# Optimization experiments

Measured on AMD Instinct MI355X. Metric: run time of the kernel, lower is better.

The kernel has to match this reference:

```python
import jax, jax.numpy as jnp
import numpy as np

N, D, K = 131072, 64, 1024


def setup_inputs() -> dict:
    key = jax.random.key(0)
    kx, kc = jax.random.split(key)
    x = jax.random.normal(kx, (N, D), dtype=jnp.float32)
    # codebook ~ trunc_normal(std=0.2); plain normal*0.2 is a faithful stand-in
    codebook = 0.2 * jax.random.normal(kc, (K, D), dtype=jnp.float32)
    temperature = jnp.ones((1,), dtype=jnp.float32)
    return {"x": x, "codebook": codebook, "temperature": temperature}


def reference(x, codebook, temperature):
    # squared euclidean distances: [N, K]
    dist = (
        jnp.sum(x * x, axis=1, keepdims=True)
        + jnp.sum(codebook * codebook, axis=1)[None, :]
        - 2.0 * (x @ codebook.T)
    )
    neg_dist = -dist
    ids = jnp.argmax(neg_dist, axis=1)  # nearest code per row
    # Note: original tests `if self.train:` (a bound method, always truthy),
    # so the gumbel-softmax branch always executes.
    gkey = jax.random.key(42)
    g = jax.random.gumbel(gkey, neg_dist.shape, dtype=neg_dist.dtype)
    weights = jax.nn.softmax((neg_dist + g) / temperature[0], axis=-1)  # [N, K]
    emb = weights @ codebook  # [N, D]
    return emb, ids
```

## Files before the change

### kernel.cpp

```cpp
#include <hip/hip_runtime.h>
#include <stdint.h>

#define N_ROWS 131072
#define DIM 64
#define K_CODES 1024

typedef __attribute__((ext_vector_type(8))) short short8;
typedef __attribute__((ext_vector_type(4))) float float4v;
typedef __attribute__((ext_vector_type(4))) uint32_t u32x4;

#define LOG2E 1.4426950408889634f
#define LOG2_LN2 -0.5287663729448977f

__device__ __forceinline__ uint32_t cvt_pk_bf16(float lo, float hi) {
    uint32_t r;
    asm("v_cvt_pk_bf16_f32 %0, %1, %2" : "=v"(r) : "v"(lo), "v"(hi));
    return r;
}
__device__ __forceinline__ uint32_t lo_pack(float fe, float fo, uint32_t h) {
    float le = fe - __uint_as_float(h << 16);
    float lo_ = fo - __uint_as_float(h & 0xffff0000u);
    return cvt_pk_bf16(le, lo_);
}
__device__ __forceinline__ float exp2_fast(float x) {
    float r; asm("v_exp_f32 %0, %1" : "=v"(r) : "v"(x)); return r;
}
__device__ __forceinline__ float log2_fast(float x) {
    float r; asm("v_log_f32 %0, %1" : "=v"(r) : "v"(x)); return r;
}

__device__ __forceinline__ void dma16(const void* g, void* l) {
    __builtin_amdgcn_global_load_lds(
        (const __attribute__((address_space(1))) uint32_t*)g,
        (__attribute__((address_space(3))) uint32_t*)l,
        16, 0, 0);
}

template<int V> struct IC { static constexpr int v = V; };

__global__ __launch_bounds__(256) void nscale_kernel(const float* __restrict__ cb,
                                                     const float* __restrict__ temp,
                                                     float* __restrict__ nsc) {
    int k = blockIdx.x * 256 + threadIdx.x;
    if (k < K_CODES) {
        const float invT = 1.0f / temp[0];
        const float* r = cb + k * DIM;
        float s = 0.f;
        #pragma unroll
        for (int j = 0; j < DIM; ++j) s = fmaf(r[j], r[j], s);
        nsc[k] = fmaf(s, -invT * LOG2E, -LOG2_LN2);
    }
}

__global__ __launch_bounds__(256) void cbimg_kernel(const float* __restrict__ cb,
                                                    const float* __restrict__ temp,
                                                    uint16_t* __restrict__ img) {
    const int tile = blockIdx.x, tid = threadIdx.x;
    const int code = tid & 31, db = (tid >> 5) * 8;
    const int k = tile * 32 + code;
    const float sc = (1.0f / temp[0]) * LOG2E;
    const float4* src = reinterpret_cast<const float4*>(cb + (size_t)k * DIM + db);
    const float4 a = src[0], b = src[1];
    uint32_t h0 = cvt_pk_bf16(a.x, a.y), h1 = cvt_pk_bf16(a.z, a.w);
    uint32_t h2 = cvt_pk_bf16(b.x, b.y), h3 = cvt_pk_bf16(b.z, b.w);
    const float sax = a.x*sc, say = a.y*sc, saz = a.z*sc, saw = a.w*sc;
    const float sbx = b.x*sc, sby = b.y*sc, sbz = b.z*sc, sbw = b.w*sc;
    uint32_t g0 = cvt_pk_bf16(sax, say), g1 = cvt_pk_bf16(saz, saw);
    uint32_t g2 = cvt_pk_bf16(sbx, sby), g3 = cvt_pk_bf16(sbz, sbw);
    u32x4 hv = {g0, g1, g2, g3};
    u32x4 lv = { lo_pack(sax,say,g0), lo_pack(saz,saw,g1),
                 lo_pack(sbx,sby,g2), lo_pack(sbz,sbw,g3) };
    uint16_t* t = img + (size_t)tile * 7168;
    *(u32x4*)&t[code*72 + db]        = hv;
    *(u32x4*)&t[2304 + code*72 + db] = lv;
    const int pc = ((code & 15) << 1) | (code >> 4);
    t[4608 + (db+0)*40 + pc] = (uint16_t)h0;
    t[4608 + (db+1)*40 + pc] = (uint16_t)(h0 >> 16);
    t[4608 + (db+2)*40 + pc] = (uint16_t)h1;
    t[4608 + (db+3)*40 + pc] = (uint16_t)(h1 >> 16);
    t[4608 + (db+4)*40 + pc] = (uint16_t)h2;
    t[4608 + (db+5)*40 + pc] = (uint16_t)(h2 >> 16);
    t[4608 + (db+6)*40 + pc] = (uint16_t)h3;
    t[4608 + (db+7)*40 + pc] = (uint16_t)(h3 >> 16);
}

__device__ __forceinline__ uint32_t rotl32(uint32_t x, uint32_t r) {
    return __builtin_amdgcn_alignbit(x, x, 32u - r);
}
__device__ __forceinline__ void tf_round4(uint32_t x0[4], uint32_t x1[4], uint32_t r) {
    #pragma unroll
    for (int i = 0; i < 4; ++i) { x0[i] += x1[i]; x1[i] = rotl32(x1[i], r); x1[i] ^= x0[i]; }
}
__device__ __forceinline__ void threefry4w_k42(const uint32_t c0[4],
                                               uint32_t o0[4], uint32_t o1[4]) {
    const uint32_t ks1 = 42u, ks2 = 0x1BD11BDAu ^ 42u;
    uint32_t x0[4], x1[4];
    #pragma unroll
    for (int i = 0; i < 4; ++i) { x0[i] = c0[i]; x1[i] = c0[i] + (1u<<26) + ks1; }
    tf_round4(x0,x1,13); tf_round4(x0,x1,15); tf_round4(x0,x1,26); tf_round4(x0,x1,6);
    #pragma unroll
    for (int i = 0; i < 4; ++i) { x0[i] += ks1; x1[i] += ks2 + 1u; }
    tf_round4(x0,x1,17); tf_round4(x0,x1,29); tf_round4(x0,x1,16); tf_round4(x0,x1,24);
    #pragma unroll
    for (int i = 0; i < 4; ++i) { x0[i] += ks2; x1[i] += 2u; }
    tf_round4(x0,x1,13); tf_round4(x0,x1,15); tf_round4(x0,x1,26); tf_round4(x0,x1,6);
    #pragma unroll
    for (int i = 0; i < 4; ++i) { x1[i] += ks1 + 3u; }
    tf_round4(x0,x1,17); tf_round4(x0,x1,29); tf_round4(x0,x1,16); tf_round4(x0,x1,24);
    #pragma unroll
    for (int i = 0; i < 4; ++i) { x0[i] += ks1; x1[i] += ks2 + 4u; }
    tf_round4(x0,x1,13); tf_round4(x0,x1,15); tf_round4(x0,x1,26); tf_round4(x0,x1,6);
    #pragma unroll
    for (int i = 0; i < 4; ++i) { o0[i] = x0[i] + ks2; o1[i] = x1[i] + 5u; }
}

__device__ __forceinline__ float gumbel_l(uint32_t bits) {
    uint32_t fb = __builtin_amdgcn_alignbit(0x7Fu, bits, 9u);
    return log2_fast(__uint_as_float(fb) - 1.0f);
}

template<bool T1>
__device__ __forceinline__ void quant_body(
    const float* __restrict__ x, const uint16_t* __restrict__ img,
    const float* __restrict__ cb, const float invT,
    float* __restrict__ out_emb, float* __restrict__ out_ids,
    char* smem, const float* __restrict__ nscg)
{
    uint16_t* const xhiP  = (uint16_t*)smem;
    uint16_t* const xloP  = (uint16_t*)(smem + 9216);
    uint16_t* const pbufP = (uint16_t*)(smem + 28672);
    float*    const nscLDS = (float*)(smem + 33792);

    const int tid  = threadIdx.x;
    const int wave = tid >> 6, lane = tid & 63, quad = lane >> 4, col = lane & 15;
    const int rowbase = blockIdx.x * 32 + wave * 8;

    {
        const int s = tid >> 2, w = s >> 4, t = s & 15, dq = tid & 3;
        const int row = blockIdx.x * 32 + w * 8 + (t >> 1) + ((t & 1) << 16);
        const float4* src = reinterpret_cast<const float4*>(x + (size_t)row * DIM + dq * 16);
        float4 f0 = src[0], f1 = src[1], f2 = src[2], f3 = src[3];
        u32x4 hA = { cvt_pk_bf16(f0.x,f0.y), cvt_pk_bf16(f0.z,f0.w),
                     cvt_pk_bf16(f1.x,f1.y), cvt_pk_bf16(f1.z,f1.w) };
        u32x4 hB = { cvt_pk_bf16(f2.x,f2.y), cvt_pk_bf16(f2.z,f2.w),
                     cvt_pk_bf16(f3.x,f3.y), cvt_pk_bf16(f3.z,f3.w) };
        u32x4 lA = { lo_pack(f0.x,f0.y,hA[0]), lo_pack(f0.z,f0.w,hA[1]),
                     lo_pack(f1.x,f1.y,hA[2]), lo_pack(f1.z,f1.w,hA[3]) };
        u32x4 lB = { lo_pack(f2.x,f2.y,hB[0]), lo_pack(f2.z,f2.w,hB[1]),
                     lo_pack(f3.x,f3.y,hB[2]), lo_pack(f3.z,f3.w,hB[3]) };
        uint16_t* dsth = &xhiP[(w*16 + t)*72 + dq*16];
        uint16_t* dstl = &xloP[(w*16 + t)*72 + dq*16];
        *(u32x4*)(dsth)     = hA;
        *(u32x4*)(dsth + 8) = hB;
        *(u32x4*)(dstl)     = lA;
        *(u32x4*)(dstl + 8) = lB;
    }
    __syncthreads();

    const int arb = (wave*16 + col)*72;
    const short8 ahi0 = *(const short8*)&xhiP[arb + quad*8];
    const short8 ahi1 = *(const short8*)&xhiP[arb + 32 + quad*8];
    const short8 alo0 = *(const short8*)&xloP[arb + quad*8];
    const short8 alo1 = *(const short8*)&xloP[arb + 32 + quad*8];
    __syncthreads();

    const char* gdma = (const char*)img + (size_t)lane * 16;
    auto dma_tile = [&](int tile, int bofs) {
        const char* s = gdma + (size_t)tile * 14336;
        char* d = smem + bofs;
        dma16(s + (size_t)wave*1024,     d + wave*1024);
        dma16(s + (size_t)(wave+4)*1024, d + (wave+4)*1024);
        dma16(s + (size_t)(wave+8)*1024, d + (wave+8)*1024);
        if (wave < 2) dma16(s + (size_t)(wave+12)*1024, d + (wave+12)*1024);
    };
    dma_tile(0, 0);
    dma16((const char*)nscg + (size_t)wave*1024 + (size_t)lane*16,
          smem + 33792 + wave*1024);
    __syncthreads();

    const uint32_t base_c0 = (uint32_t)(rowbase + 2*quad) * 1024u + (uint32_t)col;

    float m[4]  = {-1e30f, -1e30f, -1e30f, -1e30f};
    float Zp[4] = {0.f, 0.f, 0.f, 0.f};
    float4v e0 = {0,0,0,0}, e1 = {0,0,0,0}, e2 = {0,0,0,0}, e3 = {0,0,0,0};
    float zt[4] = {-3.4e38f,-3.4e38f,-3.4e38f,-3.4e38f};
    float zs[4] = {-3.4e38f,-3.4e38f,-3.4e38f,-3.4e38f};
    int   kt[4] = {0,0,0,0}, ks[4] = {0,0,0,0};

    auto body = [&](int blk, auto B) {
        constexpr int BOF = decltype(B)::v;
        const uint16_t* cbhi = (const uint16_t*)(smem + BOF);
        const uint16_t* cblo = cbhi + 2304;
        const uint16_t* cbT  = cbhi + 4608;
        const int kb  = blk * 32;
        const int kc0 = kb + col, kc1 = kc0 + 16;

        if (blk + 1 < 32) dma_tile(blk + 1, BOF ^ 14336);
        const float nsc0 = nscLDS[kc0], nsc1 = nscLDS[kc1];

        float l0c[4], l1c[4];
        {
            const uint32_t cA = base_c0 + (uint32_t)kb;
            const uint32_t c0s[4] = {cA, cA + 1024u, cA + 16u, cA + 1040u};
            uint32_t o0[4], o1[4];
            threefry4w_k42(c0s, o0, o1);
            float l[8];
            #pragma unroll
            for (int i = 0; i < 4; ++i) { l[2*i] = gumbel_l(o0[i]); l[2*i+1] = gumbel_l(o1[i]); }
            #pragma unroll
            for (int j = 0; j < 4; ++j) {
                if (T1) { l0c[j] = l[j]; l1c[j] = l[4+j]; }
                else {
                    l0c[j] = -invT * (log2_fast(-l[j])   + LOG2_LN2);
                    l1c[j] = -invT * (log2_fast(-l[4+j]) + LOG2_LN2);
                }
            }
        }

        float4v S0 = {0,0,0,0}, S1 = {0,0,0,0};
        {
            const int rb0 = col*72;
            const short8 bh0 = *(const short8*)&cbhi[rb0 + quad*8];
            const short8 bh1 = *(const short8*)&cbhi[rb0 + 32 + quad*8];
            const short8 bl0 = *(const short8*)&cblo[rb0 + quad*8];
            const short8 bl1 = *(const short8*)&cblo[rb0 + 32 + quad*8];
            S0 = __builtin_amdgcn_mfma_f32_16x16x32_bf16(ahi0, bh0, S0, 0,0,0);
            S0 = __builtin_amdgcn_mfma_f32_16x16x32_bf16(ahi1, bh1, S0, 0,0,0);
            S0 = __builtin_amdgcn_mfma_f32_16x16x32_bf16(ahi0, bl0, S0, 0,0,0);
            S0 = __builtin_amdgcn_mfma_f32_16x16x32_bf16(ahi1, bl1, S0, 0,0,0);
            S0 = __builtin_amdgcn_mfma_f32_16x16x32_bf16(alo0, bh0, S0, 0,0,0);
            S0 = __builtin_amdgcn_mfma_f32_16x16x32_bf16(alo1, bh1, S0, 0,0,0);
        }
        {
            const int rb1 = (16 + col)*72;
            const short8 bh0 = *(const short8*)&cbhi[rb1 + quad*8];
            const short8 bh1 = *(const short8*)&cbhi[rb1 + 32 + quad*8];
            const short8 bl0 = *(const short8*)&cblo[rb1 + quad*8];
            const short8 bl1 = *(const short8*)&cblo[rb1 + 32 + quad*8];
            S1 = __builtin_amdgcn_mfma_f32_16x16x32_bf16(ahi0, bh0, S1, 0,0,0);
            S1 = __builtin_amdgcn_mfma_f32_16x16x32_bf16(ahi1, bh1, S1, 0,0,0);
            S1 = __builtin_amdgcn_mfma_f32_16x16x32_bf16(ahi0, bl0, S1, 0,0,0);
            S1 = __builtin_amdgcn_mfma_f32_16x16x32_bf16(ahi1, bl1, S1, 0,0,0);
            S1 = __builtin_amdgcn_mfma_f32_16x16x32_bf16(alo0, bh0, S1, 0,0,0);
            S1 = __builtin_amdgcn_mfma_f32_16x16x32_bf16(alo1, bh1, S1, 0,0,0);
        }

        float z0v[4], z1v[4];
        #pragma unroll
        for (int j = 0; j < 4; ++j) {
            const float z0 = fmaf(S0[j], 2.0f, nsc0);
            const float z1 = fmaf(S1[j], 2.0f, nsc1);
            {   const bool c1 = z0 > zt[j], c2 = z0 > zs[j];
                const float zsn = __builtin_amdgcn_fmed3f(z0, zt[j], zs[j]);
                ks[j] = c1 ? kt[j] : (c2 ? kc0 : ks[j]);
                kt[j] = c1 ? kc0 : kt[j];
                zt[j] = fmaxf(zt[j], z0);
                zs[j] = zsn; }
            {   const bool c1 = z1 > zt[j], c2 = z1 > zs[j];
                const float zsn = __builtin_amdgcn_fmed3f(z1, zt[j], zs[j]);
                ks[j] = c1 ? kt[j] : (c2 ? kc1 : ks[j]);
                kt[j] = c1 ? kc1 : kt[j];
                zt[j] = fmaxf(zt[j], z1);
                zs[j] = zsn; }
            z0v[j] = z0; z1v[j] = z1;
        }

        if (T1) {
            #pragma unroll
            for (int j = 0; j < 4; ++j) {
                const float p0 = exp2_fast(z0v[j]) * __builtin_amdgcn_rcpf(-l0c[j]);
                const float p1 = exp2_fast(z1v[j]) * __builtin_amdgcn_rcpf(-l1c[j]);
                Zp[j] += p0 + p1;
                ((uint32_t*)pbufP)[(wave*16 + quad*4 + j)*20 + col] = cvt_pk_bf16(p0, p1);
            }
        } else {
            float a0[4], a1[4], zm[4];
            #pragma unroll
            for (int j = 0; j < 4; ++j) {
                a0[j] = z0v[j] + l0c[j];
                a1[j] = z1v[j] + l1c[j];
                zm[j] = fmaxf(a0[j], a1[j]);
            }
            float4v av;
            #pragma unroll
            for (int j = 0; j < 4; ++j) {
                float mn = fmaxf(m[j], zm[j]);
                #pragma unroll
                for (int mask = 1; mask < 16; mask <<= 1)
                    mn = fmaxf(mn, __shfl_xor(mn, mask));
                const float al = exp2_fast(m[j] - mn);
                m[j] = mn; Zp[j] *= al; av[j] = al;
            }
            e0 *= av; e1 *= av; e2 *= av; e3 *= av;
            #pragma unroll
            for (int j = 0; j < 4; ++j) {
                const float p0 = exp2_fast(a0[j] - m[j]);
                const float p1 = exp2_fast(a1[j] - m[j]);
                Zp[j] += p0 + p1;
                ((uint32_t*)pbufP)[(wave*16 + quad*4 + j)*20 + col] = cvt_pk_bf16(p0, p1);
            }
        }

        const short8 pa  = *(const short8*)&pbufP[(wave*16 + col)*40 + quad*8];
        const short8 bt0 = *(const short8*)&cbT[( 0 + col)*40 + quad*8];
        const short8 bt1 = *(const short8*)&cbT[(16 + col)*40 + quad*8];
        const short8 bt2 = *(const short8*)&cbT[(32 + col)*40 + quad*8];
        const short8 bt3 = *(const short8*)&cbT[(48 + col)*40 + quad*8];
        e0 = __builtin_amdgcn_mfma_f32_16x16x32_bf16(pa, bt0, e0, 0,0,0);
        e1 = __builtin_amdgcn_mfma_f32_16x16x32_bf16(pa, bt1, e1, 0,0,0);
        e2 = __builtin_amdgcn_mfma_f32_16x16x32_bf16(pa, bt2, e2, 0,0,0);
        e3 = __builtin_amdgcn_mfma_f32_16x16x32_bf16(pa, bt3, e3, 0,0,0);

        __syncthreads();
    };

    for (int blk = 0; blk < 32; blk += 2) {
        body(blk,     IC<0>{});
        body(blk + 1, IC<14336>{});
    }

    #pragma unroll
    for (int mask = 1; mask < 16; mask <<= 1) {
        #pragma unroll
        for (int j = 0; j < 4; ++j) Zp[j] += __shfl_xor(Zp[j], mask);
    }
    #pragma unroll
    for (int mask = 1; mask < 16; mask <<= 1) {
        #pragma unroll
        for (int j = 0; j < 4; ++j) {
            const float ozt = __shfl_xor(zt[j], mask);
            const float ozs = __shfl_xor(zs[j], mask);
            const int   okt = __shfl_xor(kt[j], mask);
            const int   oks = __shfl_xor(ks[j], mask);
            const bool mf = (zt[j] > ozt) || (zt[j] == ozt && kt[j] < okt);
            const float w1 = mf ? zt[j] : ozt;  const int wk1 = mf ? kt[j] : okt;
            const float l1 = mf ? ozt : zt[j];  const int lk1 = mf ? okt : kt[j];
            const float w2 = mf ? zs[j] : ozs;  const int wk2 = mf ? ks[j] : oks;
            const bool s1 = (l1 > w2) || (l1 == w2 && lk1 < wk2);
            zt[j] = w1; kt[j] = wk1;
            zs[j] = s1 ? l1 : w2; ks[j] = s1 ? lk1 : wk2;
        }
    }
    if (col == 0) {
        #pragma unroll
        for (int j = 0; j < 4; ++j) {
            if (zt[j] - zs[j] < 0.015f * invT) {
                const int t = quad*4 + j;
                const int row = rowbase + (t >> 1) + ((t & 1) << 16);
                const float* xr = x + (size_t)row * DIM;
                const float* cA = cb + (size_t)kt[j] * DIM;
                const float* cB = cb + (size_t)ks[j] * DIM;
                double dA = 0.0, dB = 0.0;
                for (int d = 0; d < DIM; ++d) {
                    const double xv = (double)xr[d];
                    const double av2 = (double)cA[d], bv = (double)cB[d];
                    dA = fma(av2, av2, dA); dA = fma(-2.0*xv, av2, dA);
                    dB = fma(bv,  bv,  dB); dB = fma(-2.0*xv, bv,  dB);
                }
                if (dB < dA || (dB == dA && ks[j] < kt[j])) kt[j] = ks[j];
            }
        }
    }
    #pragma unroll
    for (int j = 0; j < 4; ++j) {
        const int t = quad*4 + j;
        const int row = rowbase + (t >> 1) + ((t & 1) << 16);
        const float rZ = __builtin_amdgcn_rcpf(Zp[j]);
        out_emb[(size_t)row * DIM +      col] = e0[j] * rZ;
        out_emb[(size_t)row * DIM + 16 + col] = e1[j] * rZ;
        out_emb[(size_t)row * DIM + 32 + col] = e2[j] * rZ;
        out_emb[(size_t)row * DIM + 48 + col] = e3[j] * rZ;
        if (col == 0) out_ids[row] = (float)kt[j];
    }
}

__global__ __launch_bounds__(256) __attribute__((amdgpu_waves_per_eu(4)))
void quant_kernel(
    const float* __restrict__ x, const uint16_t* __restrict__ img,
    const float* __restrict__ cb, const float* __restrict__ temp,
    const float* __restrict__ nscg,
    float* __restrict__ out_emb, float* __restrict__ out_ids)
{
    __shared__ __align__(16) char smem[37888];
    const float invT = 1.0f / temp[0];
    if (invT == 1.0f) quant_body<true >(x, img, cb, invT, out_emb, out_ids, smem, nscg);
    else              quant_body<false>(x, img, cb, invT, out_emb, out_ids, smem, nscg);
}

extern "C" void kernel_launch(void* const* d_in, const int* in_sizes, int n_in,
                              void* d_out, int out_size, void* d_ws, size_t ws_size,
                              hipStream_t stream) {
    const float* x    = (const float*)d_in[0];
    const float* cb   = (const float*)d_in[1];
    const float* temp = (const float*)d_in[2];
    float*    nsc     = (float*)d_ws;
    uint16_t* img     = (uint16_t*)((char*)d_ws + 4096);
    float* out_emb    = (float*)d_out;
    float* out_ids    = (float*)d_out + (size_t)N_ROWS * DIM;

    nscale_kernel<<<(K_CODES + 255) / 256, 256, 0, stream>>>(cb, temp, nsc);
    cbimg_kernel<<<32, 256, 0, stream>>>(cb, temp, img);
    quant_kernel<<<N_ROWS / 64, 256, 0, stream>>>(x, img, cb, temp, nsc, out_emb, out_ids);
}
```

Baseline: 304.3 us.

## Pack codebook norms into tile padding and swizzle transposed codebook layout

Stores each code's scaled norm in the unused padding of the per-tile codebook image, so the separate norm table and its DMA into shared memory go away. The transposed codebook block drops its row padding (40 to 32) and uses an XOR swizzle to avoid bank conflicts. Together these shrink the per-tile image and the shared memory per block, which could allow more resident blocks and cuts DMA instructions. The risk is that the norm read now comes from the tile buffer and the swizzle indexing must match exactly between writer and reader.

```diff
diff --git a/kernel.cpp b/kernel.cpp
--- a/kernel.cpp
+++ b/kernel.cpp
@@ -11,6 +11,8 @@
 
 #define LOG2E 1.4426950408889634f
 #define LOG2_LN2 -0.5287663729448977f
+
+#define TILE_B 13312
 
 __device__ __forceinline__ uint32_t cvt_pk_bf16(float lo, float hi) {
     uint32_t r;
@@ -40,7 +42,7 @@
 
 __global__ __launch_bounds__(256) void nscale_kernel(const float* __restrict__ cb,
                                                      const float* __restrict__ temp,
-                                                     float* __restrict__ nsc) {
+                                                     char* __restrict__ img) {
     int k = blockIdx.x * 256 + threadIdx.x;
     if (k < K_CODES) {
         const float invT = 1.0f / temp[0];
@@ -48,7 +50,9 @@
         float s = 0.f;
         #pragma unroll
         for (int j = 0; j < DIM; ++j) s = fmaf(r[j], r[j], s);
-        nsc[k] = fmaf(s, -invT * LOG2E, -LOG2_LN2);
+        const int tile = k >> 5, code = k & 31;
+        *(float*)(img + (size_t)tile * TILE_B + code * 144 + 128) =
+            fmaf(s, -invT * LOG2E, -LOG2_LN2);
     }
 }
 
@@ -70,18 +74,18 @@
     u32x4 hv = {g0, g1, g2, g3};
     u32x4 lv = { lo_pack(sax,say,g0), lo_pack(saz,saw,g1),
                  lo_pack(sbx,sby,g2), lo_pack(sbz,sbw,g3) };
-    uint16_t* t = img + (size_t)tile * 7168;
+    uint16_t* t = img + (size_t)tile * (TILE_B / 2);
     *(u32x4*)&t[code*72 + db]        = hv;
     *(u32x4*)&t[2304 + code*72 + db] = lv;
     const int pc = ((code & 15) << 1) | (code >> 4);
-    t[4608 + (db+0)*40 + pc] = (uint16_t)h0;
-    t[4608 + (db+1)*40 + pc] = (uint16_t)(h0 >> 16);
-    t[4608 + (db+2)*40 + pc] = (uint16_t)h1;
-    t[4608 + (db+3)*40 + pc] = (uint16_t)(h1 >> 16);
-    t[4608 + (db+4)*40 + pc] = (uint16_t)h2;
-    t[4608 + (db+5)*40 + pc] = (uint16_t)(h2 >> 16);
-    t[4608 + (db+6)*40 + pc] = (uint16_t)h3;
-    t[4608 + (db+7)*40 + pc] = (uint16_t)(h3 >> 16);
+    const uint16_t hh[8] = {
+        (uint16_t)h0, (uint16_t)(h0 >> 16), (uint16_t)h1, (uint16_t)(h1 >> 16),
+        (uint16_t)h2, (uint16_t)(h2 >> 16), (uint16_t)h3, (uint16_t)(h3 >> 16) };
+    #pragma unroll
+    for (int e = 0; e < 8; ++e) {
+        const int row = db + e;
+        t[4608 + row*32 + (((pc >> 3) ^ (row & 3)) << 3) + (pc & 7)] = hh[e];
+    }
 }
 
 __device__ __forceinline__ uint32_t rotl32(uint32_t x, uint32_t r) {
@@ -123,13 +127,11 @@
 __device__ __forceinline__ void quant_body(
     const float* __restrict__ x, const uint16_t* __restrict__ img,
     const float* __restrict__ cb, const float invT,
-    float* __restrict__ out_emb, float* __restrict__ out_ids,
-    char* smem, const float* __restrict__ nscg)
+    float* __restrict__ out_emb, float* __restrict__ out_ids, char* smem)
 {
     uint16_t* const xhiP  = (uint16_t*)smem;
     uint16_t* const xloP  = (uint16_t*)(smem + 9216);
-    uint16_t* const pbufP = (uint16_t*)(smem + 28672);
-    float*    const nscLDS = (float*)(smem + 33792);
+    uint16_t* const pbufP = (uint16_t*)(smem + 26624);
 
     const int tid  = threadIdx.x;
     const int wave = tid >> 6, lane = tid & 63, quad = lane >> 4, col = lane & 15;
@@ -166,16 +168,14 @@
 
     const char* gdma = (const char*)img + (size_t)lane * 16;
     auto dma_tile = [&](int tile, int bofs) {
-        const char* s = gdma + (size_t)tile * 14336;
+        const char* s = gdma + (size_t)tile * TILE_B;
         char* d = smem + bofs;
         dma16(s + (size_t)wave*1024,     d + wave*1024);
         dma16(s + (size_t)(wave+4)*1024, d + (wave+4)*1024);
         dma16(s + (size_t)(wave+8)*1024, d + (wave+8)*1024);
-        if (wave < 2) dma16(s + (size_t)(wave+12)*1024, d + (wave+12)*1024);
+        if (wave == 0) dma16(s + 12*1024, d + 12*1024);
     };
     dma_tile(0, 0);
-    dma16((const char*)nscg + (size_t)wave*1024 + (size_t)lane*16,
-          smem + 33792 + wave*1024);
     __syncthreads();
 
     const uint32_t base_c0 = (uint32_t)(rowbase + 2*quad) * 1024u + (uint32_t)col;
@@ -195,8 +195,9 @@
         const int kb  = blk * 32;
         const int kc0 = kb + col, kc1 = kc0 + 16;
 
-        if (blk + 1 < 32) dma_tile(blk + 1, BOF ^ 14336);
-        const float nsc0 = nscLDS[kc0], nsc1 = nscLDS[kc1];
+        if (blk + 1 < 32) dma_tile(blk + 1, BOF ^ TILE_B);
+        const float nsc0 = *(const float*)&cbhi[col*72 + 64];
+        const float nsc1 = *(const float*)&cbhi[(16 + col)*72 + 64];
 
         float l0c[4], l1c[4];
         {
@@ -301,11 +302,12 @@
             }
         }
 
-        const short8 pa  = *(const short8*)&pbufP[(wave*16 + col)*40 + quad*8];
-        const short8 bt0 = *(const short8*)&cbT[( 0 + col)*40 + quad*8];
-        const short8 bt1 = *(const short8*)&cbT[(16 + col)*40 + quad*8];
-        const short8 bt2 = *(const short8*)&cbT[(32 + col)*40 + quad*8];
-        const short8 bt3 = *(const short8*)&cbT[(48 + col)*40 + quad*8];
+        const short8 pa = *(const short8*)&pbufP[(wave*16 + col)*40 + quad*8];
+        const int ts = (quad ^ (col & 3)) * 8;
+        const short8 bt0 = *(const short8*)&cbT[( 0 + col)*32 + ts];
+        const short8 bt1 = *(const short8*)&cbT[(16 + col)*32 + ts];
+        const short8 bt2 = *(const short8*)&cbT[(32 + col)*32 + ts];
+        const short8 bt3 = *(const short8*)&cbT[(48 + col)*32 + ts];
         e0 = __builtin_amdgcn_mfma_f32_16x16x32_bf16(pa, bt0, e0, 0,0,0);
         e1 = __builtin_amdgcn_mfma_f32_16x16x32_bf16(pa, bt1, e1, 0,0,0);
         e2 = __builtin_amdgcn_mfma_f32_16x16x32_bf16(pa, bt2, e2, 0,0,0);
@@ -316,7 +318,7 @@
 
     for (int blk = 0; blk < 32; blk += 2) {
         body(blk,     IC<0>{});
-        body(blk + 1, IC<14336>{});
+        body(blk + 1, IC<TILE_B>{});
     }
 
     #pragma unroll
@@ -378,13 +380,12 @@
 void quant_kernel(
     const float* __restrict__ x, const uint16_t* __restrict__ img,
     const float* __restrict__ cb, const float* __restrict__ temp,
-    const float* __restrict__ nscg,
     float* __restrict__ out_emb, float* __restrict__ out_ids)
 {
-    __shared__ __align__(16) char smem[37888];
+    __shared__ __align__(16) char smem[31744];
     const float invT = 1.0f / temp[0];
-    if (invT == 1.0f) quant_body<true >(x, img, cb, invT, out_emb, out_ids, smem, nscg);
-    else              quant_body<false>(x, img, cb, invT, out_emb, out_ids, smem, nscg);
+    if (invT == 1.0f) quant_body<true >(x, img, cb, invT, out_emb, out_ids, smem);
+    else              quant_body<false>(x, img, cb, invT, out_emb, out_ids, smem);
 }
 
 extern "C" void kernel_launch(void* const* d_in, const int* in_sizes, int n_in,
@@ -393,12 +394,11 @@
     const float* x    = (const float*)d_in[0];
     const float* cb   = (const float*)d_in[1];
     const float* temp = (const float*)d_in[2];
-    float*    nsc     = (float*)d_ws;
-    uint16_t* img     = (uint16_t*)((char*)d_ws + 4096);
+    uint16_t* img     = (uint16_t*)d_ws;
     float* out_emb    = (float*)d_out;
     float* out_ids    = (float*)d_out + (size_t)N_ROWS * DIM;
 
-    nscale_kernel<<<(K_CODES + 255) / 256, 256, 0, stream>>>(cb, temp, nsc);
+    nscale_kernel<<<(K_CODES + 255) / 256, 256, 0, stream>>>(cb, temp, (char*)img);
     cbimg_kernel<<<32, 256, 0, stream>>>(cb, temp, img);
-    quant_kernel<<<N_ROWS / 64, 256, 0, stream>>>(x, img, cb, temp, nsc, out_emb, out_ids);
-}
+    quant_kernel<<<N_ROWS / 64, 256, 0, stream>>>(x, img, cb, temp, out_emb, out_ids);
+}
```

New measurement: 304.0 us. No clear change (-0.1%).
